# Kernel optimization log

Hardware: AMD Instinct MI355X
Metric: run time of the kernel (lower is better)

Reference implementation:

```python
import jax, jax.numpy as jnp
import numpy as np

N_NODES = 50000
N_EDGES = 800000
IN_DIM = 128
HID_DIM = 128
OUT_DIM = 128
THRESH = 0.05
SCALE = 50.0
EPS = 1e-6


def _graph_conv(src, dst, feat, W, b):
    """DGL GraphConv with norm='both': D_out^{-1/2} -> sum-aggregate -> D_in^{-1/2} -> linear."""
    N = feat.shape[0]
    ones = jnp.ones(src.shape[0], feat.dtype)
    deg_out = jax.ops.segment_sum(ones, src, num_segments=N)
    deg_in = jax.ops.segment_sum(ones, dst, num_segments=N)
    norm_src = jax.lax.rsqrt(jnp.maximum(deg_out, 1.0))
    norm_dst = jax.lax.rsqrt(jnp.maximum(deg_in, 1.0))
    h = feat * norm_src[:, None]                       # [N, d]
    agg = jax.ops.segment_sum(h[src], dst, num_segments=N)  # SpMM: gather + scatter-add
    return (agg * norm_dst[:, None]) @ W + b


def _gnn(src, dst, x, W1, b1, W2, b2):
    h = jax.nn.relu(_graph_conv(src, dst, x, W1, b1))
    return _graph_conv(src, dst, h, W2, b2)


def _corr(z1, z2):
    # torch .std uses ddof=1 (unbiased)
    z1s = (z1 - z1.mean(axis=0)) / (jnp.std(z1, axis=0, ddof=1) + EPS)
    z2s = (z2 - z2.mean(axis=0)) / (jnp.std(z2, axis=0, ddof=1) + EPS)
    return (z1s.T @ z2s) / z1.shape[0]


def setup_inputs() -> dict:
    key = jax.random.key(0)
    ks = jax.random.split(key, 8)
    x1 = jax.random.normal(ks[0], (N_NODES, IN_DIM), jnp.float32)
    x2 = jax.random.normal(ks[1], (N_NODES, IN_DIM), jnp.float32)
    src1 = jax.random.randint(ks[2], (N_EDGES,), 0, N_NODES, jnp.int32)
    dst1 = jax.random.randint(ks[3], (N_EDGES,), 0, N_NODES, jnp.int32)
    src2 = jax.random.randint(ks[4], (N_EDGES,), 0, N_NODES, jnp.int32)
    dst2 = jax.random.randint(ks[5], (N_EDGES,), 0, N_NODES, jnp.int32)
    W1 = jax.random.normal(ks[6], (IN_DIM, HID_DIM), jnp.float32) / np.sqrt(IN_DIM)
    W2 = jax.random.normal(ks[7], (HID_DIM, OUT_DIM), jnp.float32) / np.sqrt(HID_DIM)
    return {
        "x1": x1, "x2": x2,
        "src1": src1, "dst1": dst1, "src2": src2, "dst2": dst2,
        "W1": W1, "b1": jnp.zeros((HID_DIM,), jnp.float32),
        "W2": W2, "b2": jnp.zeros((OUT_DIM,), jnp.float32),
        "row_offsets": jnp.zeros((OUT_DIM,), jnp.float32),
        "col_offsets": jnp.zeros((OUT_DIM,), jnp.float32),
    }


def reference(x1, x2, src1, dst1, src2, dst2, W1, b1, W2, b2, row_offsets, col_offsets):
    z1 = _gnn(src1, dst1, x1, W1, b1, W2, b2)
    z2 = _gnn(src2, dst2, x2, W1, b1, W2, b2)
    C = _corr(z1, z2)                                  # [D, D]
    row_score = jnp.abs(C).mean(axis=1)
    col_score = jnp.abs(C).mean(axis=0)
    row_mask = jax.nn.sigmoid(SCALE * (row_score + row_offsets - THRESH))
    col_mask = jax.nn.sigmoid(SCALE * (col_score + col_offsets - THRESH))
    C_masked = C * (row_mask[:, None] * col_mask[None, :])
    return (C_masked, row_mask, col_mask, z1, z2)
```

## Files before the change

kernel.cpp:

```cpp
#include <hip/hip_runtime.h>

#define D 128
#define THRESH 0.05f
#define SCALE 50.0f
#define EPS 1e-6f
#define GP 48
#define CSPLIT 4
#define RPB 1088
#define NP2 52224
#define CAP 60
#define PS 2
#define NRANGE 4
#define BB 48
#define RMAX 12500
#define RNGP 12512

typedef __attribute__((ext_vector_type(4))) int i4v;
typedef __attribute__((ext_vector_type(4))) float f4v;
typedef _Float16 h8v __attribute__((ext_vector_type(8)));
typedef _Float16 h4v __attribute__((ext_vector_type(4)));

__device__ inline float4 ntload4(const float* p) {
    f4v v = __builtin_nontemporal_load((const f4v*)p);
    return make_float4(v.x, v.y, v.z, v.w);
}

__device__ inline void decode_grq(int bid, int& g, int& r, int& q) {
    g = bid >= (NRANGE * BB);
    int rem = g ? bid - NRANGE * BB : bid;
    r = rem & (NRANGE - 1);
    q = rem >> 2;
}

__global__ void __launch_bounds__(256) count_kernel(const int* __restrict__ src1,
                                                    const int* __restrict__ dst1,
                                                    const int* __restrict__ src2,
                                                    const int* __restrict__ dst2,
                                                    unsigned int* __restrict__ staging,
                                                    int E, int N) {
    __shared__ unsigned int cnt[RMAX];
    int g, r, q;
    decode_grq(blockIdx.x, g, r, q);
    const int* __restrict__ src = g ? src2 : src1;
    const int* __restrict__ dst = g ? dst2 : dst1;

    int rng = (N + NRANGE - 1) / NRANGE;
    int lo = r * rng;
    int hi = min(N, lo + rng);
    int nr = hi - lo;
    int seg = (E + BB - 1) / BB;
    int s0 = q * seg;
    int s1 = min(E, s0 + seg);
    int tid = threadIdx.x;

    for (int i = tid; i < nr; i += 256) cnt[i] = 0u;
    __syncthreads();

    for (int e = s0 + tid * 4; e < s1; e += 1024) {
        int ss[4], dd[4];
        if (e + 4 <= s1) {
            i4v a = *(const i4v*)(src + e);
            i4v b = *(const i4v*)(dst + e);
            ss[0] = a.x; ss[1] = a.y; ss[2] = a.z; ss[3] = a.w;
            dd[0] = b.x; dd[1] = b.y; dd[2] = b.z; dd[3] = b.w;
        } else {
#pragma unroll
            for (int c = 0; c < 4; ++c) {
                int ee = e + c;
                ss[c] = (ee < s1) ? src[ee] : -1;
                dd[c] = (ee < s1) ? dst[ee] : -1;
            }
        }
#pragma unroll
        for (int c = 0; c < 4; ++c) {
            int s = ss[c], d = dd[c];
            if (s >= lo && s < hi) atomicAdd(&cnt[s - lo], 1u);
            if (d >= lo && d < hi) atomicAdd(&cnt[d - lo], 0x10000u);
        }
    }
    __syncthreads();

    unsigned int* row = staging + (size_t)(((g * NRANGE + r) * BB) + q) * RNGP;
    for (int i = tid; i < nr; i += 256) row[i] = cnt[i];
}

__global__ void scan_kernel(unsigned int* __restrict__ staging, int* __restrict__ pad1,
                            int* __restrict__ pad2, int N) {
    int t = blockIdx.x * 256 + threadIdx.x;
    if (t >= 2 * N) return;
    int g = t >= N;
    int d = g ? t - N : t;
    int rng = (N + NRANGE - 1) / NRANGE;
    int r = d / rng;
    int i = d - r * rng;
    int* __restrict__ pad = g ? pad2 : pad1;

    unsigned int* base = staging + (size_t)((g * NRANGE + r) * BB) * RNGP + i;
    unsigned int oc = 0, run = 0;
#pragma unroll 4
    for (int q = 0; q < BB; ++q) {
        unsigned int c = base[(size_t)q * RNGP];
        base[(size_t)q * RNGP] = run;
        oc += c & 0xFFFFu;
        run += c >> 16;
    }
    pad[d * PS] = (int)oc;
    pad[d * PS + 1] = (int)run;
}

__global__ void __launch_bounds__(256) place_kernel(const int* __restrict__ src1,
                                                    const int* __restrict__ dst1,
                                                    const int* __restrict__ src2,
                                                    const int* __restrict__ dst2,
                                                    const unsigned int* __restrict__ staging,
                                                    unsigned short* __restrict__ bucket1,
                                                    unsigned short* __restrict__ bucket2,
                                                    int E, int N) {
    __shared__ unsigned int cur[RMAX];
    int g, r, q;
    decode_grq(blockIdx.x, g, r, q);
    const int* __restrict__ src = g ? src2 : src1;
    const int* __restrict__ dst = g ? dst2 : dst1;
    unsigned short* __restrict__ bucket = g ? bucket2 : bucket1;

    int rng = (N + NRANGE - 1) / NRANGE;
    int lo = r * rng;
    int hi = min(N, lo + rng);
    int nr = hi - lo;
    int seg = (E + BB - 1) / BB;
    int s0 = q * seg;
    int s1 = min(E, s0 + seg);
    int tid = threadIdx.x;

    const unsigned int* row = staging + (size_t)(((g * NRANGE + r) * BB) + q) * RNGP;
    for (int i = tid; i < nr; i += 256) cur[i] = row[i];
    __syncthreads();

    for (int e = s0 + tid * 4; e < s1; e += 1024) {
        int ss[4], dd[4];
        if (e + 4 <= s1) {
            i4v a = *(const i4v*)(src + e);
            i4v b = *(const i4v*)(dst + e);
            ss[0] = a.x; ss[1] = a.y; ss[2] = a.z; ss[3] = a.w;
            dd[0] = b.x; dd[1] = b.y; dd[2] = b.z; dd[3] = b.w;
        } else {
#pragma unroll
            for (int c = 0; c < 4; ++c) {
                int ee = e + c;
                ss[c] = (ee < s1) ? src[ee] : -1;
                dd[c] = (ee < s1) ? dst[ee] : -1;
            }
        }
#pragma unroll
        for (int c = 0; c < 4; ++c) {
            int s = ss[c], d = dd[c];
            if (d >= lo && d < hi) {
                unsigned int pos = atomicAdd(&cur[d - lo], 1u);
                if (pos < CAP) bucket[(size_t)d * CAP + pos] = (unsigned short)s;
            }
        }
    }
}

__global__ void wtrans_kernel(const float* __restrict__ W1, const float* __restrict__ W2,
                              _Float16* __restrict__ Wt1, _Float16* __restrict__ Wt2,
                              _Float16* __restrict__ y1, _Float16* __restrict__ y2, int N) {
    if (blockIdx.x == 2 * D * D / 256) {
        int t = threadIdx.x;
        if (t < D) y1[(size_t)N * D + t] = (_Float16)0;
        else y2[(size_t)N * D + (t - D)] = (_Float16)0;
        return;
    }
    int e = blockIdx.x * 256 + threadIdx.x;
    int h = e >= D * D;
    int rem = h ? e - D * D : e;
    int j = rem >> 7, k = rem & 127;
    const float* W = h ? W2 : W1;
    _Float16* Wt = h ? Wt2 : Wt1;
    Wt[j * D + k] = (_Float16)W[k * D + j];
}

template <bool F32IN>
__global__ void __launch_bounds__(256) gemm_ns(const float* __restrict__ tf1,
                                               const float* __restrict__ tf2,
                                               const _Float16* __restrict__ th1,
                                               const _Float16* __restrict__ th2,
                                               const int* __restrict__ pad1,
                                               const int* __restrict__ pad2,
                                               const _Float16* __restrict__ Wt,
                                               _Float16* __restrict__ y1,
                                               _Float16* __restrict__ y2, int N) {
    __shared__ _Float16 sA[128 * D];
    __shared__ _Float16 sB[D * D];
    int g = blockIdx.y;
    const float* tf = g ? tf2 : tf1;
    const _Float16* th = g ? th2 : th1;
    const int* pad = g ? pad2 : pad1;
    _Float16* y = g ? y2 : y1;
    int tid = threadIdx.x;
    int row0 = blockIdx.x * 128;

#pragma unroll
    for (int q = 0; q < 8; ++q) {
        int c = q * 256 + tid;
        int j = c >> 4, u = c & 15;
        h8v v = *(const h8v*)(Wt + j * D + u * 8);
        int byte = j * 256 + ((u * 16) ^ ((j & 7) << 4));
        *(h8v*)((char*)sB + byte) = v;
    }
#pragma unroll
    for (int q = 0; q < 8; ++q) {
        int c = q * 256 + tid;
        int row = c >> 4, u = c & 15;
        int gr = row0 + row;
        h8v hv = {};
        if (gr < N) {
            if (F32IN) {
                float nsv = rsqrtf(fmaxf((float)pad[gr * PS], 1.f));
                const float* p = tf + (size_t)gr * D + u * 8;
                float4 v0 = *(const float4*)p;
                float4 v1 = *(const float4*)(p + 4);
                hv[0] = (_Float16)(v0.x * nsv); hv[1] = (_Float16)(v0.y * nsv);
                hv[2] = (_Float16)(v0.z * nsv); hv[3] = (_Float16)(v0.w * nsv);
                hv[4] = (_Float16)(v1.x * nsv); hv[5] = (_Float16)(v1.y * nsv);
                hv[6] = (_Float16)(v1.z * nsv); hv[7] = (_Float16)(v1.w * nsv);
            } else {
                hv = *(const h8v*)(th + (size_t)gr * D + u * 8);
            }
        }
        int byte = row * 256 + ((u * 16) ^ ((row & 7) << 4));
        *(h8v*)((char*)sA + byte) = hv;
    }
    __syncthreads();

    int w = tid >> 6;
    int l = tid & 63;
    int l16 = l & 15, lg = l >> 4;
    f4v acc[2][8];
#pragma unroll
    for (int m = 0; m < 2; ++m)
#pragma unroll
        for (int n = 0; n < 8; ++n) acc[m][n] = (f4v){0.f, 0.f, 0.f, 0.f};

#pragma unroll
    for (int kc = 0; kc < 4; ++kc) {
        h8v a[2];
#pragma unroll
        for (int m = 0; m < 2; ++m) {
            int row = w * 32 + m * 16 + l16;
            int u = kc * 4 + lg;
            int byte = row * 256 + ((u * 16) ^ ((row & 7) << 4));
            a[m] = *(const h8v*)((const char*)sA + byte);
        }
#pragma unroll
        for (int n = 0; n < 8; ++n) {
            int j = n * 16 + l16;
            int u = kc * 4 + lg;
            int byte = j * 256 + ((u * 16) ^ ((j & 7) << 4));
            h8v b = *(const h8v*)((const char*)sB + byte);
#pragma unroll
            for (int m = 0; m < 2; ++m)
                acc[m][n] = __builtin_amdgcn_mfma_f32_16x16x32_f16(a[m], b, acc[m][n], 0, 0, 0);
        }
    }

#pragma unroll
    for (int m = 0; m < 2; ++m) {
        int rbase = row0 + w * 32 + m * 16 + lg * 4;
#pragma unroll
        for (int n = 0; n < 8; ++n) {
            int col = n * 16 + l16;
#pragma unroll
            for (int r = 0; r < 4; ++r) {
                int row = rbase + r;
                if (row < N) y[(size_t)row * D + col] = (_Float16)acc[m][n][r];
            }
        }
    }
}

template <bool OUT16>
__global__ void __launch_bounds__(512, 8) gather_kernel(
        const unsigned short* __restrict__ bucket1,
        const unsigned short* __restrict__ bucket2,
        const int* __restrict__ pad1, const int* __restrict__ pad2,
        const _Float16* __restrict__ y1, const _Float16* __restrict__ y2,
        const float* __restrict__ bias,
        float* __restrict__ zf1, float* __restrict__ zf2,
        _Float16* __restrict__ zh1, _Float16* __restrict__ zh2, int N) {
    int g = blockIdx.y;
    const unsigned short* bucket = g ? bucket2 : bucket1;
    const int* pad = g ? pad2 : pad1;
    const _Float16* y = g ? y2 : y1;
    float* zf = g ? zf2 : zf1;
    _Float16* zh = g ? zh2 : zh1;

    int wave = threadIdx.x >> 6;
    int lane = threadIdx.x & 63;
    int node = blockIdx.x * 8 + wave;
    if (node >= N) return;
    int deg = pad[node * PS + 1];
    int cnt = min(deg, CAP);
    float ndv = rsqrtf(fmaxf((float)deg, 1.f));
    int sid = N;
    if (lane < cnt) sid = bucket[(size_t)node * CAP + lane];
    int grp = lane >> 4;
    int sl = lane & 15;
    const _Float16* yp = y + sl * 8;
    const h8v vone = {(_Float16)1, (_Float16)1, (_Float16)1, (_Float16)1,
                      (_Float16)1, (_Float16)1, (_Float16)1, (_Float16)1};
    float acc[8] = {0.f, 0.f, 0.f, 0.f, 0.f, 0.f, 0.f, 0.f};
    for (int j = 0; j < cnt; j += 16) {
        int cmax = cnt - j;
        h8v v[4];
#pragma unroll
        for (int c = 0; c < 4; ++c) {
            if (c * 4 < cmax) {
                int idx = j + c * 4 + grp;
                int s = __shfl(sid, idx);
                s = (idx < cnt) ? s : N;
                v[c] = *(const h8v*)(yp + ((unsigned)s << 7));
            }
        }
#pragma unroll
        for (int c = 0; c < 4; ++c) {
            if (c * 4 < cmax) {
#pragma unroll
                for (int u = 0; u < 8; ++u)
                    acc[u] += (float)v[c][u] * (float)vone[u];
            }
        }
    }
#pragma unroll
    for (int u = 0; u < 8; ++u) {
        acc[u] += __shfl_xor(acc[u], 16);
        acc[u] += __shfl_xor(acc[u], 32);
    }
    if (grp == 0) {
        float4 b0 = *(const float4*)(bias + sl * 8);
        float4 b1 = *(const float4*)(bias + sl * 8 + 4);
        float o[8];
        o[0] = acc[0] * ndv + b0.x; o[1] = acc[1] * ndv + b0.y;
        o[2] = acc[2] * ndv + b0.z; o[3] = acc[3] * ndv + b0.w;
        o[4] = acc[4] * ndv + b1.x; o[5] = acc[5] * ndv + b1.y;
        o[6] = acc[6] * ndv + b1.z; o[7] = acc[7] * ndv + b1.w;
        if (OUT16) {
            float nsv = rsqrtf(fmaxf((float)pad[node * PS], 1.f));
            h8v hv;
#pragma unroll
            for (int u = 0; u < 8; ++u) hv[u] = (_Float16)(fmaxf(o[u], 0.f) * nsv);
            *(h8v*)(zh + (size_t)node * D + sl * 8) = hv;
        } else {
            *(float4*)(zf + (size_t)node * D + sl * 8) = make_float4(o[0], o[1], o[2], o[3]);
            *(float4*)(zf + (size_t)node * D + sl * 8 + 4) = make_float4(o[4], o[5], o[6], o[7]);
        }
    }
}

__global__ void __launch_bounds__(256) ztrans_kernel(const float* __restrict__ z1,
                                                     const float* __restrict__ z2,
                                                     _Float16* __restrict__ zt1,
                                                     _Float16* __restrict__ zt2, int N) {
    __shared__ _Float16 tile[64][132];
    int g = blockIdx.y;
    const float* z = g ? z2 : z1;
    _Float16* zt = g ? zt2 : zt1;
    int n0 = blockIdx.x * 64;
    int tid = threadIdx.x;
#pragma unroll
    for (int it = 0; it < 8; ++it) {
        int idx = it * 256 + tid;
        int row = idx >> 5;
        int c4 = (idx & 31) * 4;
        int gr = n0 + row;
        float4 v = make_float4(0.f, 0.f, 0.f, 0.f);
        if (gr < N) v = *(const float4*)&z[(size_t)gr * D + c4];
        h4v h = {(_Float16)v.x, (_Float16)v.y, (_Float16)v.z, (_Float16)v.w};
        *(h4v*)&tile[row][c4] = h;
    }
    __syncthreads();
    int col = tid >> 1, half = tid & 1;
    _Float16 buf[32];
#pragma unroll
    for (int k = 0; k < 32; ++k) buf[k] = tile[half * 32 + k][col];
    _Float16* dst = zt + (size_t)col * NP2 + n0 + half * 32;
#pragma unroll
    for (int c = 0; c < 4; ++c) *(h8v*)(dst + c * 8) = *(const h8v*)&buf[c * 8];
}

__global__ void __launch_bounds__(512) gram_mfma(const _Float16* __restrict__ zt1,
                                                 const _Float16* __restrict__ zt2,
                                                 float* __restrict__ part,
                                                 float* __restrict__ statpart) {
    int tid = threadIdx.x;
    int w = tid >> 6, l = tid & 63;
    int l16 = l & 15, lg = l >> 4;
    int cy = blockIdx.y * 32;
    f4v acc[2];
    acc[0] = (f4v){0.f, 0.f, 0.f, 0.f};
    acc[1] = (f4v){0.f, 0.f, 0.f, 0.f};
    float sA = 0.f, qA = 0.f, sB = 0.f, qB = 0.f;
    int r0 = blockIdx.x * RPB;
    const _Float16* ap = zt1 + (size_t)(w * 16 + l16) * NP2 + lg * 8;
    const _Float16* bp0 = zt2 + (size_t)(cy + l16) * NP2 + lg * 8;
    const _Float16* bp1 = zt2 + (size_t)(cy + 16 + l16) * NP2 + lg * 8;
#pragma unroll 1
    for (int ks = 0; ks < RPB / 32; ++ks) {
        int k0 = r0 + ks * 32;
        h8v a = *(const h8v*)(ap + k0);
        h8v b0 = *(const h8v*)(bp0 + k0);
        h8v b1 = *(const h8v*)(bp1 + k0);
        if (blockIdx.y == 0) {
#pragma unroll
            for (int j = 0; j < 8; ++j) {
                float f = (float)a[j];
                sA += f;
                qA += f * f;
            }
        }
        if (w < 2) {
            h8v bb = w ? b1 : b0;
#pragma unroll
            for (int j = 0; j < 8; ++j) {
                float f = (float)bb[j];
                sB += f;
                qB += f * f;
            }
        }
        acc[0] = __builtin_amdgcn_mfma_f32_16x16x32_f16(a, b0, acc[0], 0, 0, 0);
        acc[1] = __builtin_amdgcn_mfma_f32_16x16x32_f16(a, b1, acc[1], 0, 0, 0);
    }
    float* pb = part + (size_t)blockIdx.x * (D * D);
#pragma unroll
    for (int n = 0; n < 2; ++n)
#pragma unroll
        for (int r = 0; r < 4; ++r)
            pb[(w * 16 + lg * 4 + r) * D + cy + n * 16 + l16] = acc[n][r];
    float* sp = statpart + (size_t)blockIdx.x * 512;
    if (blockIdx.y == 0) {
        sA += __shfl_xor(sA, 16); sA += __shfl_xor(sA, 32);
        qA += __shfl_xor(qA, 16); qA += __shfl_xor(qA, 32);
        if (lg == 0) {
            int row = w * 16 + l16;
            sp[row] = sA;
            sp[D + row] = qA;
        }
    }
    if (w < 2) {
        sB += __shfl_xor(sB, 16); sB += __shfl_xor(sB, 32);
        qB += __shfl_xor(qB, 16); qB += __shfl_xor(qB, 32);
        if (lg == 0) {
            int col = cy + w * 16 + l16;
            sp[2 * D + col] = sB;
            sp[3 * D + col] = qB;
        }
    }
}

__global__ void reduce_part(const float* __restrict__ part, float* __restrict__ Csum) {
    int e = blockIdx.x * 256 + threadIdx.x;
    float s = 0.f;
#pragma unroll 8
    for (int p = 0; p < GP; ++p)
        s += __builtin_nontemporal_load(&part[(size_t)p * (D * D) + e]);
    Csum[e] = s;
}

__global__ void __launch_bounds__(1024) corrmask_kernel(const float* __restrict__ Csum,
                                                        const float* __restrict__ statpart,
                                                        const float* __restrict__ roff,
                                                        const float* __restrict__ coff,
                                                        float* __restrict__ out, int N) {
    __shared__ float cL[D * D];
    __shared__ float statsh[512];
    __shared__ float m1s[D], i1s[D], m2s[D], i2s[D];
    __shared__ float rowpart[D][2];
    __shared__ float colpart[8][D];
    __shared__ float rms[D], cms[D];
    int t = threadIdx.x;
    int j = t & 127, rg = t >> 7;
    if (t < 512) {
        float s = 0.f;
        for (int p = 0; p < GP; ++p) s += statpart[(size_t)p * 512 + t];
        statsh[t] = s;
    }
    __syncthreads();
    float fn = (float)N;
    if (t < D) {
        float m1 = statsh[t] / fn;
        float v1 = fmaxf((statsh[D + t] - fn * m1 * m1) / (fn - 1.f), 0.f);
        m1s[t] = m1;
        i1s[t] = 1.f / (sqrtf(v1) + EPS);
    } else if (t < 2 * D) {
        int jj = t - D;
        float m2 = statsh[2 * D + jj] / fn;
        float v2 = fmaxf((statsh[3 * D + jj] - fn * m2 * m2) / (fn - 1.f), 0.f);
        m2s[jj] = m2;
        i2s[jj] = 1.f / (sqrtf(v2) + EPS);
    }
    __syncthreads();
    float b = m2s[j], vj = i2s[j];
    float invfn = 1.f / fn;
    float colacc = 0.f;
    for (int k = 0; k < 16; ++k) {
        int i = rg * 16 + k;
        int e = i * D + j;
        float c = (Csum[e] - fn * m1s[i] * b) * (i1s[i] * vj) * invfn;
        cL[e] = c;
        float a = fabsf(c);
        colacc += a;
        for (int o = 1; o < 64; o <<= 1) a += __shfl_xor(a, o);
        if ((j & 63) == 0) rowpart[i][j >> 6] = a;
    }
    colpart[rg][j] = colacc;
    __syncthreads();
    if (t < D) {
        float rs = rowpart[t][0] + rowpart[t][1];
        float rm = 1.f / (1.f + expf(-SCALE * (rs / (float)D + roff[t] - THRESH)));
        rms[t] = rm;
        out[D * D + t] = rm;
    } else if (t < 2 * D) {
        int jj = t - D;
        float cs = 0.f;
#pragma unroll
        for (int g2 = 0; g2 < 8; ++g2) cs += colpart[g2][jj];
        float cm = 1.f / (1.f + expf(-SCALE * (cs / (float)D + coff[jj] - THRESH)));
        cms[jj] = cm;
        out[D * D + D + jj] = cm;
    }
    __syncthreads();
    for (int k = 0; k < 16; ++k) {
        int i = rg * 16 + k;
        int e = i * D + j;
        out[e] = cL[e] * rms[i] * cms[j];
    }
}

extern "C" void kernel_launch(void* const* d_in, const int* in_sizes, int n_in,
                              void* d_out, int out_size, void* d_ws, size_t ws_size,
                              hipStream_t stream) {
    const float* x1 = (const float*)d_in[0];
    const float* x2 = (const float*)d_in[1];
    const int* src1 = (const int*)d_in[2];
    const int* dst1 = (const int*)d_in[3];
    const int* src2 = (const int*)d_in[4];
    const int* dst2 = (const int*)d_in[5];
    const float* W1 = (const float*)d_in[6];
    const float* b1 = (const float*)d_in[7];
    const float* W2 = (const float*)d_in[8];
    const float* b2 = (const float*)d_in[9];
    const float* roff = (const float*)d_in[10];
    const float* coff = (const float*)d_in[11];

    const int N = in_sizes[0] / D;
    const int E = in_sizes[2];

    float* ws = (float*)d_ws;
    unsigned int* staging = (unsigned int*)ws;
    unsigned short* bucket1 =
        (unsigned short*)(staging + (size_t)2 * NRANGE * BB * RNGP);
    unsigned short* bucket2 = bucket1 + (size_t)N * CAP;
    int* pad1 = (int*)(bucket2 + (size_t)N * CAP);
    int* pad2 = pad1 + (size_t)N * PS;
    _Float16* Wt1 = (_Float16*)(pad2 + (size_t)N * PS);
    _Float16* Wt2 = Wt1 + D * D;
    _Float16* y1 = Wt2 + D * D;
    _Float16* y2 = y1 + (size_t)(N + 1) * D;
    _Float16* zt1 = (_Float16*)ws;
    _Float16* zt2 = zt1 + (size_t)D * NP2;
    float* part = (float*)(zt2 + (size_t)D * NP2);
    float* Csum = part + (size_t)GP * D * D;
    float* statpart = Csum + D * D;

    float* out = (float*)d_out;
    float* z1 = out + D * D + 2 * D;
    float* z2 = z1 + (size_t)N * D;
    _Float16* hp1 = (_Float16*)z1;
    _Float16* hp2 = (_Float16*)z2;

    count_kernel<<<2 * NRANGE * BB, 256, 0, stream>>>(src1, dst1, src2, dst2, staging, E, N);
    scan_kernel<<<(2 * N + 255) / 256, 256, 0, stream>>>(staging, pad1, pad2, N);
    place_kernel<<<2 * NRANGE * BB, 256, 0, stream>>>(src1, dst1, src2, dst2, staging,
                                                      bucket1, bucket2, E, N);
    wtrans_kernel<<<2 * D * D / 256 + 1, 256, 0, stream>>>(W1, W2, Wt1, Wt2, y1, y2, N);

    const int gblk = (N + 127) / 128;
    {
        dim3 gg(gblk, 2), ga((N + 7) / 8, 2);
        gemm_ns<true><<<gg, 256, 0, stream>>>(x1, x2, nullptr, nullptr, pad1, pad2,
                                              Wt1, y1, y2, N);
        gather_kernel<true><<<ga, 512, 0, stream>>>(bucket1, bucket2, pad1, pad2, y1, y2,
                                                    b1, nullptr, nullptr, hp1, hp2, N);
        gemm_ns<false><<<gg, 256, 0, stream>>>(nullptr, nullptr, hp1, hp2, pad1, pad2,
                                               Wt2, y1, y2, N);
        gather_kernel<false><<<ga, 512, 0, stream>>>(bucket1, bucket2, pad1, pad2, y1, y2,
                                                     b2, z1, z2, nullptr, nullptr, N);
    }

    {
        dim3 tgrid(NP2 / 64, 2);
        ztrans_kernel<<<tgrid, 256, 0, stream>>>(z1, z2, zt1, zt2, N);
    }
    {
        dim3 ggrid(GP, CSPLIT);
        gram_mfma<<<ggrid, 512, 0, stream>>>(zt1, zt2, part, statpart);
    }
    reduce_part<<<64, 256, 0, stream>>>(part, Csum);
    corrmask_kernel<<<1, 1024, 0, stream>>>(Csum, statpart, roff, coff, out, N);
}
```

Baseline: 257.9 us.

## Split gather feature columns into four 32-wide slices across blockIdx.x

The gather kernel now splits the 128 feature columns into four 32-column slices, each handled by a separate block, with the graph index and slice packed into blockIdx.x and the node group in blockIdx.y. Each wave now handles 16 edges per iteration, with 4 lanes covering 64 bytes of a source row, instead of 4 edges with 16 lanes covering the full 256-byte row. Consecutive blocks then share the same node rows but touch different column slices, which is meant to improve cache locality and memory-level parallelism. The cost is that neighbor indices and degree are reloaded four times per node, and the reduction needs two extra shuffle steps.

```diff
diff --git a/kernel.cpp b/kernel.cpp
--- a/kernel.cpp
+++ b/kernel.cpp
@@ -288,7 +288,9 @@
         const float* __restrict__ bias,
         float* __restrict__ zf1, float* __restrict__ zf2,
         _Float16* __restrict__ zh1, _Float16* __restrict__ zh2, int N) {
-    int g = blockIdx.y;
+    int grpid = blockIdx.x;
+    int g = grpid >> 2;
+    int cg = grpid & 3;
     const unsigned short* bucket = g ? bucket2 : bucket1;
     const int* pad = g ? pad2 : pad1;
     const _Float16* y = g ? y2 : y1;
@@ -297,48 +299,40 @@
 
     int wave = threadIdx.x >> 6;
     int lane = threadIdx.x & 63;
-    int node = blockIdx.x * 8 + wave;
+    int node = blockIdx.y * 8 + wave;
     if (node >= N) return;
     int deg = pad[node * PS + 1];
     int cnt = min(deg, CAP);
     float ndv = rsqrtf(fmaxf((float)deg, 1.f));
     int sid = N;
-    if (lane < cnt) sid = bucket[(size_t)node * CAP + lane];
-    int grp = lane >> 4;
-    int sl = lane & 15;
-    const _Float16* yp = y + sl * 8;
+    if (lane < cnt)
+        sid = __builtin_nontemporal_load(&bucket[(size_t)node * CAP + lane]);
+    int equad = lane >> 2;
+    int cq = lane & 3;
+    int coff = cg * 32 + cq * 8;
+    const _Float16* yp = y + coff;
     const h8v vone = {(_Float16)1, (_Float16)1, (_Float16)1, (_Float16)1,
                       (_Float16)1, (_Float16)1, (_Float16)1, (_Float16)1};
     float acc[8] = {0.f, 0.f, 0.f, 0.f, 0.f, 0.f, 0.f, 0.f};
     for (int j = 0; j < cnt; j += 16) {
-        int cmax = cnt - j;
-        h8v v[4];
-#pragma unroll
-        for (int c = 0; c < 4; ++c) {
-            if (c * 4 < cmax) {
-                int idx = j + c * 4 + grp;
-                int s = __shfl(sid, idx);
-                s = (idx < cnt) ? s : N;
-                v[c] = *(const h8v*)(yp + ((unsigned)s << 7));
-            }
-        }
-#pragma unroll
-        for (int c = 0; c < 4; ++c) {
-            if (c * 4 < cmax) {
-#pragma unroll
-                for (int u = 0; u < 8; ++u)
-                    acc[u] += (float)v[c][u] * (float)vone[u];
-            }
-        }
+        int idx = j + equad;
+        int s = __shfl(sid, idx & 63);
+        s = (idx < cnt) ? s : N;
+        h8v v = *(const h8v*)(yp + ((unsigned)s << 7));
+#pragma unroll
+        for (int u = 0; u < 8; ++u)
+            acc[u] += (float)v[u] * (float)vone[u];
     }
 #pragma unroll
     for (int u = 0; u < 8; ++u) {
+        acc[u] += __shfl_xor(acc[u], 4);
+        acc[u] += __shfl_xor(acc[u], 8);
         acc[u] += __shfl_xor(acc[u], 16);
         acc[u] += __shfl_xor(acc[u], 32);
     }
-    if (grp == 0) {
-        float4 b0 = *(const float4*)(bias + sl * 8);
-        float4 b1 = *(const float4*)(bias + sl * 8 + 4);
+    if (equad == 0) {
+        float4 b0 = *(const float4*)(bias + coff);
+        float4 b1 = *(const float4*)(bias + coff + 4);
         float o[8];
         o[0] = acc[0] * ndv + b0.x; o[1] = acc[1] * ndv + b0.y;
         o[2] = acc[2] * ndv + b0.z; o[3] = acc[3] * ndv + b0.w;
@@ -349,10 +343,10 @@
             h8v hv;
 #pragma unroll
             for (int u = 0; u < 8; ++u) hv[u] = (_Float16)(fmaxf(o[u], 0.f) * nsv);
-            *(h8v*)(zh + (size_t)node * D + sl * 8) = hv;
+            *(h8v*)(zh + (size_t)node * D + coff) = hv;
         } else {
-            *(float4*)(zf + (size_t)node * D + sl * 8) = make_float4(o[0], o[1], o[2], o[3]);
-            *(float4*)(zf + (size_t)node * D + sl * 8 + 4) = make_float4(o[4], o[5], o[6], o[7]);
+            *(float4*)(zf + (size_t)node * D + coff) = make_float4(o[0], o[1], o[2], o[3]);
+            *(float4*)(zf + (size_t)node * D + coff + 4) = make_float4(o[4], o[5], o[6], o[7]);
         }
     }
 }
@@ -586,7 +580,7 @@
 
     const int gblk = (N + 127) / 128;
     {
-        dim3 gg(gblk, 2), ga((N + 7) / 8, 2);
+        dim3 gg(gblk, 2), ga(8, (N + 7) / 8);
         gemm_ns<true><<<gg, 256, 0, stream>>>(x1, x2, nullptr, nullptr, pad1, pad2,
                                               Wt1, y1, y2, N);
         gather_kernel<true><<<ga, 512, 0, stream>>>(bucket1, bucket2, pad1, pad2, y1, y2,
```

Measured after the change: 476.7 us. 1.85x slower.
